# Performance work log

Hardware: AMD Instinct MI355X
Metric: run time of the kernel (lower is better)

The kernel has to match this reference:

```python
import jax, jax.numpy as jnp
import numpy as np

D_MODEL = 768
NHEAD = 12
D_K = D_MODEL // NHEAD
D_FF = 3072
EPS = 1e-6


def layer_norm(x, a, b):
    # torch LayerNorm here: mean/std over last dim, std is UNBIASED (n-1), eps added to std
    n = x.shape[-1]
    m = jnp.mean(x, axis=-1, keepdims=True)
    var = jnp.sum((x - m) ** 2, axis=-1, keepdims=True) / (n - 1)
    return a * (x - m) / (jnp.sqrt(var) + EPS) + b


def setup_inputs() -> dict:
    key = jax.random.key(0)
    ks = jax.random.split(key, 12)
    B, S = 2, 2048
    s = 1.0 / np.sqrt(D_MODEL)
    inp = {
        'x': jax.random.normal(ks[0], (B, S, D_MODEL), jnp.float32),
        'mask': jnp.ones((B, 1, S), jnp.int32),
        'Wq': jax.random.normal(ks[1], (D_MODEL, D_MODEL), jnp.float32) * s,
        'bq': jnp.zeros((D_MODEL,), jnp.float32),
        'Wk': jax.random.normal(ks[2], (D_MODEL, D_MODEL), jnp.float32) * s,
        'bk': jnp.zeros((D_MODEL,), jnp.float32),
        'Wv': jax.random.normal(ks[3], (D_MODEL, D_MODEL), jnp.float32) * s,
        'bv': jnp.zeros((D_MODEL,), jnp.float32),
        'Wo': jax.random.normal(ks[4], (D_MODEL, D_MODEL), jnp.float32) * s,
        'bo': jnp.zeros((D_MODEL,), jnp.float32),
        'ln1_a': jnp.ones((D_MODEL,), jnp.float32),
        'ln1_b': jnp.zeros((D_MODEL,), jnp.float32),
        'W1': jax.random.normal(ks[5], (D_MODEL, D_FF), jnp.float32) * s,
        'b1': jnp.zeros((D_FF,), jnp.float32),
        'W2': jax.random.normal(ks[6], (D_FF, D_MODEL), jnp.float32) * (1.0 / np.sqrt(D_FF)),
        'b2': jnp.zeros((D_MODEL,), jnp.float32),
        'ln2_a': jnp.ones((D_MODEL,), jnp.float32),
        'ln2_b': jnp.zeros((D_MODEL,), jnp.float32),
    }
    return inp


def reference(x, mask, Wq, bq, Wk, bk, Wv, bv, Wo, bo, ln1_a, ln1_b, W1, b1, W2, b2, ln2_a, ln2_b):
    B, S, _ = x.shape
    # --- sublayer 1: pre-norm self-attention + residual (dropout = eval/no-op) ---
    h = layer_norm(x, ln1_a, ln1_b)
    q = (h @ Wq + bq).reshape(B, S, NHEAD, D_K).transpose(0, 2, 1, 3)  # [B,H,S,Dk]
    k = (h @ Wk + bk).reshape(B, S, NHEAD, D_K).transpose(0, 2, 1, 3)
    v = (h @ Wv + bv).reshape(B, S, NHEAD, D_K).transpose(0, 2, 1, 3)
    scores = jnp.einsum('bhqd,bhkd->bhqk', q, k) / np.sqrt(D_K)  # [B,H,S,S]
    scores = jnp.where(mask[:, None] == 0, jnp.float32(-1e9), scores)
    attn = jax.nn.softmax(scores, axis=-1)
    ctx = jnp.einsum('bhqk,bhkd->bhqd', attn, v)  # [B,H,S,Dk]
    ctx = ctx.transpose(0, 2, 1, 3).reshape(B, S, D_MODEL)
    x = x + (ctx @ Wo + bo)
    # --- sublayer 2: pre-norm FFN + residual ---
    h2 = layer_norm(x, ln2_a, ln2_b)
    ff = jax.nn.relu(h2 @ W1 + b1) @ W2 + b2
    return x + ff
```

## Files before the change

kernel.cpp:

```cpp
#include <hip/hip_runtime.h>
#include <hip/hip_bf16.h>
#include <stdint.h>

#define DM 768
#define DFF 3072
#define NH 12
#define DK 64
#define SS 2048
#define NTOK 4096
#define KCH 2

typedef __hip_bfloat16 bf16;
typedef short bf16x8 __attribute__((ext_vector_type(8)));
typedef float f32x4 __attribute__((ext_vector_type(4)));

#define MFMA16(a, b, c) __builtin_amdgcn_mfma_f32_16x16x32_bf16((a), (b), (c), 0, 0, 0)

#define QSCALE 0.18033688011112042f

#if __has_builtin(__builtin_amdgcn_exp2f)
#define EXP2F(x) __builtin_amdgcn_exp2f(x)
#else
#define EXP2F(x) exp2f(x)
#endif

static __device__ __forceinline__ bf16 f2b(float f) { return __float2bfloat16(f); }
static __device__ __forceinline__ unsigned short f2b_bits(float f) {
    bf16 h = __float2bfloat16(f);
    return *reinterpret_cast<unsigned short*>(&h);
}
static __device__ __forceinline__ float b2f(bf16 h) { return __bfloat162float(h); }

static __device__ __forceinline__ void g2l16(const void* g, void* l) {
    __builtin_amdgcn_global_load_lds(
        (const __attribute__((address_space(1))) unsigned int*)g,
        (__attribute__((address_space(3))) unsigned int*)(uintptr_t)l,
        16, 0, 0);
}

__global__ __launch_bounds__(256) void fused_pre(const float* Wq, const float* Wk,
                                                 const float* Wv, const float* Wo,
                                                 const float* W1, const float* W2,
                                                 bf16* WqT, bf16* WkT, bf16* WvT,
                                                 bf16* WoT, bf16* W1T, bf16* W2T,
                                                 const float* __restrict__ x,
                                                 const float* __restrict__ lg,
                                                 const float* __restrict__ lb,
                                                 bf16* __restrict__ hout) {
    int id = blockIdx.x;
    if (id >= 6912) {
        int wid = threadIdx.x >> 6, lane = threadIdx.x & 63;
        int row = (id - 6912) * 4 + wid;
        const float* xr = x + (size_t)row * DM;
        float v[12];
        float s = 0.f;
#pragma unroll
        for (int i = 0; i < 12; ++i) { v[i] = xr[lane + i * 64]; s += v[i]; }
#pragma unroll
        for (int off = 32; off >= 1; off >>= 1) s += __shfl_xor(s, off);
        float mean = s * (1.f / 768.f);
        float s2 = 0.f;
#pragma unroll
        for (int i = 0; i < 12; ++i) { float d = v[i] - mean; s2 += d * d; }
#pragma unroll
        for (int off = 32; off >= 1; off >>= 1) s2 += __shfl_xor(s2, off);
        float rstd = 1.f / (sqrtf(s2 * (1.f / 767.f)) + 1e-6f);
        bf16* orow = hout + (size_t)row * DM;
#pragma unroll
        for (int i = 0; i < 12; ++i) {
            int c = lane + i * 64;
            orow[c] = f2b(lg[c] * (v[i] - mean) * rstd + lb[c]);
        }
        return;
    }
    __shared__ float tile[32][33];
    const float* W; bf16* WT; int K, N, n0, k0;
    if (id < 2304) {
        int z = id / 576, r = id % 576;
        W  = (z == 0) ? Wq : (z == 1) ? Wk : (z == 2) ? Wv : Wo;
        WT = (z == 0) ? WqT : (z == 1) ? WkT : (z == 2) ? WvT : WoT;
        K = 768; N = 768; n0 = (r % 24) * 32; k0 = (r / 24) * 32;
    } else if (id < 4608) {
        int r = id - 2304; W = W1; WT = W1T;
        K = 768; N = 3072; n0 = (r % 96) * 32; k0 = (r / 96) * 32;
    } else {
        int r = id - 4608; W = W2; WT = W2T;
        K = 3072; N = 768; n0 = (r % 24) * 32; k0 = (r / 24) * 32;
    }
    int tx = threadIdx.x & 31, ty = threadIdx.x >> 5;
#pragma unroll
    for (int r = ty; r < 32; r += 8)
        tile[r][tx] = W[(size_t)(k0 + r) * N + n0 + tx];
    __syncthreads();
#pragma unroll
    for (int r = ty; r < 32; r += 8)
        WT[(size_t)(n0 + r) * K + k0 + tx] = f2b(tile[tx][r]);
}

__global__ __launch_bounds__(256) void ln_fwd(const float* __restrict__ x,
                                              const float* __restrict__ g,
                                              const float* __restrict__ be,
                                              bf16* __restrict__ out) {
    int wid = threadIdx.x >> 6, lane = threadIdx.x & 63;
    int row = blockIdx.x * 4 + wid;
    const float* xr = x + (size_t)row * DM;
    float v[12];
    float s = 0.f;
#pragma unroll
    for (int i = 0; i < 12; ++i) { v[i] = xr[lane + i * 64]; s += v[i]; }
#pragma unroll
    for (int off = 32; off >= 1; off >>= 1) s += __shfl_xor(s, off);
    float mean = s * (1.f / 768.f);
    float s2 = 0.f;
#pragma unroll
    for (int i = 0; i < 12; ++i) { float d = v[i] - mean; s2 += d * d; }
#pragma unroll
    for (int off = 32; off >= 1; off >>= 1) s2 += __shfl_xor(s2, off);
    float rstd = 1.f / (sqrtf(s2 * (1.f / 767.f)) + 1e-6f);
    bf16* orow = out + (size_t)row * DM;
#pragma unroll
    for (int i = 0; i < 12; ++i) {
        int c = lane + i * 64;
        orow[c] = f2b(g[c] * (v[i] - mean) * rstd + be[c]);
    }
}

__device__ __forceinline__ void gemm_core(const bf16* __restrict__ A,
                                          const bf16* __restrict__ BT,
                                          int K, int bm, int bn,
                                          bf16* As, bf16* Bs,
                                          f32x4 acc[4][4]) {
    int tid = threadIdx.x;
    int lane = tid & 63, quad = lane >> 4, lid = lane & 15;
    int wid = tid >> 6;
    int wm = (wid >> 1) * 64, wn = (wid & 1) * 64;
    int s0 = tid, s1 = tid + 256;
    int r0 = s0 >> 2, c0 = (s0 & 3) ^ ((r0 >> 1) & 3);
    int r1 = s1 >> 2, c1 = (s1 & 3) ^ ((r1 >> 1) & 3);
    const bf16* A0 = A + (size_t)(bm + r0) * K + c0 * 8;
    const bf16* A1 = A + (size_t)(bm + r1) * K + c1 * 8;
    const bf16* B0 = BT + (size_t)(bn + r0) * K + c0 * 8;
    const bf16* B1 = BT + (size_t)(bn + r1) * K + c1 * 8;
    int rdc = quad ^ ((lid >> 1) & 3);
    g2l16(A0, As + s0 * 8);
    g2l16(B0, Bs + s0 * 8);
    g2l16(A1, As + s1 * 8);
    g2l16(B1, Bs + s1 * 8);
    for (int k0 = 0; k0 < K; k0 += 32) {
        __syncthreads();
        int cur = (k0 >> 5) & 1;
        if (k0 + 32 < K) {
            int nb = (cur ^ 1) * 4096;
            g2l16(A0 + k0 + 32, As + nb + s0 * 8);
            g2l16(B0 + k0 + 32, Bs + nb + s0 * 8);
            g2l16(A1 + k0 + 32, As + nb + s1 * 8);
            g2l16(B1 + k0 + 32, Bs + nb + s1 * 8);
        }
        const bf16* Ac = As + cur * 4096;
        const bf16* Bc = Bs + cur * 4096;
        bf16x8 af[4], bfr[4];
#pragma unroll
        for (int i = 0; i < 4; ++i) af[i]  = *(const bf16x8*)&Ac[(wm + i * 16 + lid) * 32 + rdc * 8];
#pragma unroll
        for (int j = 0; j < 4; ++j) bfr[j] = *(const bf16x8*)&Bc[(wn + j * 16 + lid) * 32 + rdc * 8];
#pragma unroll
        for (int i = 0; i < 4; ++i)
#pragma unroll
            for (int j = 0; j < 4; ++j)
                acc[i][j] = MFMA16(af[i], bfr[j], acc[i][j]);
    }
}

__global__ __launch_bounds__(256) void gemm_qkv(const bf16* __restrict__ A,
                                                const bf16* __restrict__ WqT,
                                                const bf16* __restrict__ WkT,
                                                const bf16* __restrict__ WvT,
                                                const float* __restrict__ bq,
                                                const float* __restrict__ bk,
                                                const float* __restrict__ bv,
                                                bf16* __restrict__ qb,
                                                bf16* __restrict__ kb,
                                                bf16* __restrict__ vtb) {
    __shared__ bf16 As[2 * 128 * 32];
    __shared__ bf16 Bs[2 * 128 * 32];
    int which = blockIdx.x / 6;
    int bn = (blockIdx.x % 6) * 128;
    int bm = blockIdx.y * 128;
    const bf16* BT = (which == 0) ? WqT : (which == 1) ? WkT : WvT;
    const float* bias = (which == 0) ? bq : (which == 1) ? bk : bv;
    f32x4 acc[4][4] = {};
    gemm_core(A, BT, DM, bm, bn, As, Bs, acc);

    int tid = threadIdx.x, wid = tid >> 6, lane = tid & 63, quad = lane >> 4, lid = lane & 15;
    int wm = (wid >> 1) * 64, wn = (wid & 1) * 64;
    float sc = (which == 0) ? QSCALE : 1.f;
#pragma unroll
    for (int j = 0; j < 4; ++j) {
        int col = bn + wn + j * 16 + lid;
        float bb = bias[col];
        int hh = col >> 6, d = col & 63;
#pragma unroll
        for (int i = 0; i < 4; ++i) {
            int rowbase = bm + wm + i * 16 + quad * 4;
            int b = rowbase >> 11;
            int s0 = rowbase & 2047;
            if (which == 2) {
                ushort4 pk;
                pk.x = f2b_bits(acc[i][j][0] + bb);
                pk.y = f2b_bits(acc[i][j][1] + bb);
                pk.z = f2b_bits(acc[i][j][2] + bb);
                pk.w = f2b_bits(acc[i][j][3] + bb);
                *(ushort4*)&vtb[(((size_t)b * NH + hh) * DK + d) * SS + s0] = pk;
            } else {
                bf16* dst = which ? kb : qb;
#pragma unroll
                for (int r = 0; r < 4; ++r)
                    dst[(((size_t)b * NH + hh) * SS + (s0 + r)) * DK + d] = f2b((acc[i][j][r] + bb) * sc);
            }
        }
    }
}

template <int EPI>
__global__ __launch_bounds__(256) void gemm_ep(const bf16* __restrict__ A,
                                               const bf16* __restrict__ BT,
                                               const float* __restrict__ bias,
                                               const float* __restrict__ res,
                                               void* __restrict__ outp,
                                               int N, int K) {
    __shared__ bf16 As[2 * 128 * 32];
    __shared__ bf16 Bs[2 * 128 * 32];
    int bm = blockIdx.y * 128, bn = blockIdx.x * 128;
    f32x4 acc[4][4] = {};
    gemm_core(A, BT, K, bm, bn, As, Bs, acc);

    int tid = threadIdx.x, wid = tid >> 6, lane = tid & 63, quad = lane >> 4, lid = lane & 15;
    int wm = (wid >> 1) * 64, wn = (wid & 1) * 64;
#pragma unroll
    for (int j = 0; j < 4; ++j) {
        int col = bn + wn + j * 16 + lid;
        float bb = bias[col];
#pragma unroll
        for (int i = 0; i < 4; ++i) {
#pragma unroll
            for (int r = 0; r < 4; ++r) {
                int row = bm + wm + i * 16 + quad * 4 + r;
                float v = acc[i][j][r] + bb;
                if (EPI == 2) {
                    ((float*)outp)[(size_t)row * N + col] = res[(size_t)row * N + col] + v;
                } else {
                    ((bf16*)outp)[(size_t)row * N + col] = f2b(fmaxf(v, 0.f));
                }
            }
        }
    }
}

template <int EPI>
__global__ __launch_bounds__(256) void gemm_ep96(const bf16* __restrict__ A,
                                                 const bf16* __restrict__ BT,
                                                 const float* __restrict__ bias,
                                                 const float* __restrict__ res,
                                                 void* __restrict__ outp,
                                                 int N, int K) {
    __shared__ bf16 As[2 * 64 * 32];
    __shared__ bf16 Bs[2 * 96 * 32];
    int bm = blockIdx.y * 64, bn = blockIdx.x * 96;
    int tid = threadIdx.x, wid = tid >> 6, lane = tid & 63, quad = lane >> 4, lid = lane & 15;
    int wm = (wid >> 1) * 32, wn = (wid & 1) * 48;
    f32x4 acc[2][3] = {};
    int ra = tid >> 2, ca = (tid & 3) ^ ((ra >> 1) & 3);
    int s0 = tid, s1 = tid + 256;
    int rb0 = s0 >> 2, cb0 = (s0 & 3) ^ ((rb0 >> 1) & 3);
    int rb1 = s1 >> 2, cb1 = (s1 & 3) ^ ((rb1 >> 1) & 3);
    const bf16* Ap = A + (size_t)(bm + ra) * K + ca * 8;
    const bf16* B0 = BT + (size_t)(bn + rb0) * K + cb0 * 8;
    const bf16* B1 = BT + (size_t)(bn + rb1) * K + cb1 * 8;
    int rdc = quad ^ ((lid >> 1) & 3);
    bool doB1 = tid < 128;
    g2l16(Ap, As + tid * 8);
    g2l16(B0, Bs + s0 * 8);
    if (doB1) g2l16(B1, Bs + s1 * 8);
    for (int k0 = 0; k0 < K; k0 += 32) {
        __syncthreads();
        int cur = (k0 >> 5) & 1;
        if (k0 + 32 < K) {
            g2l16(Ap + k0 + 32, As + (cur ^ 1) * 2048 + tid * 8);
            g2l16(B0 + k0 + 32, Bs + (cur ^ 1) * 3072 + s0 * 8);
            if (doB1) g2l16(B1 + k0 + 32, Bs + (cur ^ 1) * 3072 + s1 * 8);
        }
        const bf16* Ac = As + cur * 2048;
        const bf16* Bc = Bs + cur * 3072;
        bf16x8 af[2], bfr[3];
#pragma unroll
        for (int i = 0; i < 2; ++i) af[i]  = *(const bf16x8*)&Ac[(wm + i * 16 + lid) * 32 + rdc * 8];
#pragma unroll
        for (int j = 0; j < 3; ++j) bfr[j] = *(const bf16x8*)&Bc[(wn + j * 16 + lid) * 32 + rdc * 8];
#pragma unroll
        for (int i = 0; i < 2; ++i)
#pragma unroll
            for (int j = 0; j < 3; ++j)
                acc[i][j] = MFMA16(af[i], bfr[j], acc[i][j]);
    }
#pragma unroll
    for (int j = 0; j < 3; ++j) {
        int col = bn + wn + j * 16 + lid;
        float bb = bias[col];
#pragma unroll
        for (int i = 0; i < 2; ++i) {
#pragma unroll
            for (int r = 0; r < 4; ++r) {
                int row = bm + wm + i * 16 + quad * 4 + r;
                float v = acc[i][j][r] + bb;
                if (EPI == 2) {
                    ((float*)outp)[(size_t)row * N + col] = res[(size_t)row * N + col] + v;
                } else {
                    ((bf16*)outp)[(size_t)row * N + col] = f2b(fmaxf(v, 0.f));
                }
            }
        }
    }
}

__global__ __launch_bounds__(256) void attn_part(const bf16* __restrict__ qb,
                                                 const bf16* __restrict__ kb,
                                                 const bf16* __restrict__ vtb,
                                                 const int* __restrict__ mask,
                                                 bf16* __restrict__ part,
                                                 float* __restrict__ lws) {
    __shared__ bf16 Ks[2 * 64 * 64];
    __shared__ bf16 VTs[2 * 64 * 64];
    __shared__ bf16 Ps[128 * 72];
    int bh = blockIdx.y;
    int b = bh / NH;
    int q0 = blockIdx.x * 128;
    int kc = blockIdx.z;
    const bf16* Kp = kb  + (size_t)bh * SS * DK;
    const bf16* VT = vtb + (size_t)bh * DK * SS;
    int tid = threadIdx.x, wid = tid >> 6, lane = tid & 63, quad = lane >> 4, lid = lane & 15;

    int s0 = tid, s1 = tid + 256;
    int r0 = s0 >> 3, c0 = (s0 & 7) ^ (r0 & 7);
    int r1 = s1 >> 3, c1 = (s1 & 7) ^ (r1 & 7);

    const int* mrow = mask + b * SS;
    int tbeg = kc * (SS / 64 / KCH), tend = (kc + 1) * (SS / 64 / KCH);

    int myfull;
    {
        const int4* m4 = (const int4*)(mrow + tbeg * 64);
        int4 mm = m4[tid];
        myfull = (mm.x != 0) & (mm.y != 0) & (mm.z != 0) & (mm.w != 0);
    }
    int blockfull = __syncthreads_and(myfull);

    bf16x8 qf0[2], qf1[2];
#pragma unroll
    for (int u = 0; u < 2; ++u) {
        const bf16* Qrow = qb + ((size_t)bh * SS + q0 + wid * 32 + u * 16 + lid) * DK;
        qf0[u] = *(const bf16x8*)&Qrow[quad * 8];
        qf1[u] = *(const bf16x8*)&Qrow[32 + quad * 8];
    }

    bf16x8 ones;
#pragma unroll
    for (int i = 0; i < 8; ++i) ones[i] = (short)0x3F80;

    int rdc  = quad ^ (lid & 7);
    int rdc2 = rdc ^ 4;

    f32x4 accv[2][4] = {};
    f32x4 accl[2] = {};

    {
        int k0 = tbeg * 64;
        g2l16(Kp + (size_t)(k0 + r0) * DK + c0 * 8, Ks + s0 * 8);
        g2l16(Kp + (size_t)(k0 + r1) * DK + c1 * 8, Ks + s1 * 8);
        g2l16(VT + (size_t)r0 * SS + k0 + c0 * 8, VTs + s0 * 8);
        g2l16(VT + (size_t)r1 * SS + k0 + c1 * 8, VTs + s1 * 8);
    }

    int cur = 0;
    for (int t = tbeg; t < tend; ++t) {
        int k0 = t * 64;
        __syncthreads();
        if (t + 1 < tend) {
            int k0n = (t + 1) * 64;
            int nb = (cur ^ 1) * 4096;
            g2l16(Kp + (size_t)(k0n + r0) * DK + c0 * 8, Ks + nb + s0 * 8);
            g2l16(Kp + (size_t)(k0n + r1) * DK + c1 * 8, Ks + nb + s1 * 8);
            g2l16(VT + (size_t)r0 * SS + k0n + c0 * 8, VTs + nb + s0 * 8);
            g2l16(VT + (size_t)r1 * SS + k0n + c1 * 8, VTs + nb + s1 * 8);
        }
        const bf16* Kc  = Ks  + cur * 4096;
        const bf16* VTc = VTs + cur * 4096;

#pragma unroll
        for (int ns = 0; ns < 4; ++ns) {
            bf16x8 kf0 = *(const bf16x8*)&Kc[(ns * 16 + lid) * 64 + rdc * 8];
            bf16x8 kf1 = *(const bf16x8*)&Kc[(ns * 16 + lid) * 64 + rdc2 * 8];
#pragma unroll
            for (int u = 0; u < 2; ++u) {
                f32x4 st = {};
                st = MFMA16(kf0, qf0[u], st);
                st = MFMA16(kf1, qf1[u], st);
                float p0, p1, p2, p3;
                if (blockfull) {
                    p0 = EXP2F(st[0]);
                    p1 = EXP2F(st[1]);
                    p2 = EXP2F(st[2]);
                    p3 = EXP2F(st[3]);
                } else {
                    int4 mk = *(const int4*)&mrow[k0 + ns * 16 + quad * 4];
                    p0 = mk.x ? EXP2F(st[0]) : 0.f;
                    p1 = mk.y ? EXP2F(st[1]) : 0.f;
                    p2 = mk.z ? EXP2F(st[2]) : 0.f;
                    p3 = mk.w ? EXP2F(st[3]) : 0.f;
                }
                __hip_bfloat162 h01 = __float22bfloat162_rn(make_float2(p0, p1));
                __hip_bfloat162 h23 = __float22bfloat162_rn(make_float2(p2, p3));
                uint2 pw;
                pw.x = *(unsigned int*)&h01;
                pw.y = *(unsigned int*)&h23;
                *(uint2*)&Ps[(wid * 32 + u * 16 + lid) * 72 + ns * 16 + quad * 4] = pw;
            }
        }

        bf16x8 pa0[2], pa1[2];
#pragma unroll
        for (int u = 0; u < 2; ++u) {
            pa0[u] = *(const bf16x8*)&Ps[(wid * 32 + u * 16 + lid) * 72 + quad * 8];
            pa1[u] = *(const bf16x8*)&Ps[(wid * 32 + u * 16 + lid) * 72 + 32 + quad * 8];
            accl[u] = MFMA16(pa0[u], ones, accl[u]);
            accl[u] = MFMA16(pa1[u], ones, accl[u]);
        }

#pragma unroll
        for (int ds = 0; ds < 4; ++ds) {
            bf16x8 vf0 = *(const bf16x8*)&VTc[(ds * 16 + lid) * 64 + rdc * 8];
            bf16x8 vf1 = *(const bf16x8*)&VTc[(ds * 16 + lid) * 64 + rdc2 * 8];
#pragma unroll
            for (int u = 0; u < 2; ++u) {
                accv[u][ds] = MFMA16(pa0[u], vf0, accv[u][ds]);
                accv[u][ds] = MFMA16(pa1[u], vf1, accv[u][ds]);
            }
        }
        cur ^= 1;
    }

    bf16* pb = part + ((size_t)kc * (2 * NH) + bh) * DK * SS;
#pragma unroll
    for (int u = 0; u < 2; ++u) {
        if (lid == 0) {
#pragma unroll
            for (int r = 0; r < 4; ++r)
                lws[((size_t)kc * (2 * NH) + bh) * SS + q0 + wid * 32 + u * 16 + quad * 4 + r] = accl[u][r];
        }
        int qbase = q0 + wid * 32 + u * 16 + quad * 4;
#pragma unroll
        for (int ds = 0; ds < 4; ++ds) {
            int d = ds * 16 + lid;
            ushort4 pk;
            pk.x = f2b_bits(accv[u][ds][0]);
            pk.y = f2b_bits(accv[u][ds][1]);
            pk.z = f2b_bits(accv[u][ds][2]);
            pk.w = f2b_bits(accv[u][ds][3]);
            *(ushort4*)&pb[(size_t)d * SS + qbase] = pk;
        }
    }
}

__global__ __launch_bounds__(256) void attn_combine(const bf16* __restrict__ part,
                                                    const float* __restrict__ lws,
                                                    bf16* __restrict__ ctx) {
    __shared__ float tile[64][66];
    __shared__ float linv[64];
    int bh = blockIdx.y;
    int b = bh / NH, h = bh % NH;
    int q0 = blockIdx.x * 64;
    int tid = threadIdx.x;

    if (tid < 64) {
        float l = 0.f;
#pragma unroll
        for (int kc = 0; kc < KCH; ++kc)
            l += lws[((size_t)kc * (2 * NH) + bh) * SS + q0 + tid];
        linv[tid] = 1.f / l;
    }

    int d = tid >> 2, qs = (tid & 3) * 16;
    const bf16* p0 = part + (((size_t)0 * (2 * NH) + bh) * DK + d) * SS + q0 + qs;
    const bf16* p1 = part + (((size_t)1 * (2 * NH) + bh) * DK + d) * SS + q0 + qs;
    bf16x8 a0 = *(const bf16x8*)p0;
    bf16x8 a1 = *(const bf16x8*)(p0 + 8);
    bf16x8 b0 = *(const bf16x8*)p1;
    bf16x8 b1 = *(const bf16x8*)(p1 + 8);
#pragma unroll
    for (int i = 0; i < 8; ++i) {
        tile[d][qs + i]     = b2f(((const bf16*)&a0)[i]) + b2f(((const bf16*)&b0)[i]);
        tile[d][qs + 8 + i] = b2f(((const bf16*)&a1)[i]) + b2f(((const bf16*)&b1)[i]);
    }
    __syncthreads();

    int q = tid >> 2, ds2 = (tid & 3) * 16;
    float rl = linv[q];
    unsigned int wv[8];
#pragma unroll
    for (int i = 0; i < 8; ++i) {
        __hip_bfloat162 hh = __float22bfloat162_rn(
            make_float2(tile[ds2 + 2 * i][q] * rl, tile[ds2 + 2 * i + 1][q] * rl));
        wv[i] = *(unsigned int*)&hh;
    }
    bf16* crow = ctx + (size_t)(b * SS + q0 + q) * DM + h * DK + ds2;
    uint4 u0 = {wv[0], wv[1], wv[2], wv[3]};
    uint4 u1 = {wv[4], wv[5], wv[6], wv[7]};
    *(uint4*)&crow[0] = u0;
    *(uint4*)&crow[8] = u1;
}

extern "C" void kernel_launch(void* const* d_in, const int* in_sizes, int n_in,
                              void* d_out, int out_size, void* d_ws, size_t ws_size,
                              hipStream_t stream) {
    const float* x    = (const float*)d_in[0];
    const int*   mask = (const int*)d_in[1];
    const float* Wq   = (const float*)d_in[2];
    const float* bq   = (const float*)d_in[3];
    const float* Wk   = (const float*)d_in[4];
    const float* bk   = (const float*)d_in[5];
    const float* Wv   = (const float*)d_in[6];
    const float* bv   = (const float*)d_in[7];
    const float* Wo   = (const float*)d_in[8];
    const float* bo   = (const float*)d_in[9];
    const float* ln1a = (const float*)d_in[10];
    const float* ln1b = (const float*)d_in[11];
    const float* W1   = (const float*)d_in[12];
    const float* b1   = (const float*)d_in[13];
    const float* W2   = (const float*)d_in[14];
    const float* b2   = (const float*)d_in[15];
    const float* ln2a = (const float*)d_in[16];
    const float* ln2b = (const float*)d_in[17];
    float* out = (float*)d_out;

    char* w = (char*)d_ws;
    bf16* h   = (bf16*)w; w += (size_t)NTOK * DM * 2;
    bf16* qb  = (bf16*)w; w += (size_t)NTOK * DM * 2;
    bf16* kb  = (bf16*)w; w += (size_t)NTOK * DM * 2;
    bf16* vtb = (bf16*)w; w += (size_t)NTOK * DM * 2;
    bf16* ctx = (bf16*)w; w += (size_t)NTOK * DM * 2;
    bf16* h2  = (bf16*)w; w += (size_t)NTOK * DM * 2;
    bf16* ffa = (bf16*)w; w += (size_t)NTOK * DFF * 2;
    float* x1 = (float*)w; w += (size_t)NTOK * DM * 4;
    bf16* WqT = (bf16*)w; w += (size_t)DM * DM * 2;
    bf16* WkT = (bf16*)w; w += (size_t)DM * DM * 2;
    bf16* WvT = (bf16*)w; w += (size_t)DM * DM * 2;
    bf16* WoT = (bf16*)w; w += (size_t)DM * DM * 2;
    bf16* W1T = (bf16*)w; w += (size_t)DM * DFF * 2;
    bf16* W2T = (bf16*)w; w += (size_t)DM * DFF * 2;

    bf16*  part = ffa;
    float* lws  = x1;

    fused_pre<<<6912 + NTOK / 4, 256, 0, stream>>>(Wq, Wk, Wv, Wo, W1, W2,
                                                   WqT, WkT, WvT, WoT, W1T, W2T,
                                                   x, ln1a, ln1b, h);
    gemm_qkv<<<dim3(18, 32), 256, 0, stream>>>(h, WqT, WkT, WvT, bq, bk, bv, qb, kb, vtb);
    attn_part<<<dim3(SS / 128, 2 * NH, KCH), 256, 0, stream>>>(qb, kb, vtb, mask, part, lws);
    attn_combine<<<dim3(SS / 64, 2 * NH), 256, 0, stream>>>(part, lws, ctx);
    gemm_ep96<2><<<dim3(8, 64), 256, 0, stream>>>(ctx, WoT, bo, x, (void*)x1, DM, DM);
    ln_fwd<<<NTOK / 4, 256, 0, stream>>>(x1, ln2a, ln2b, h2);
    gemm_ep<3><<<dim3(24, 32), 256, 0, stream>>>(h2, W1T, b1, nullptr, (void*)ffa, DFF, DM);
    gemm_ep96<2><<<dim3(8, 64), 256, 0, stream>>>(ffa, W2T, b2, x1, (void*)out, DM, DFF);
}
```

Before: 287.0 us.

## Retile QKV GEMM, add split-K W2 GEMM, and XCD-swizzle block order

The QKV projection now uses 128x96 tiles with an inlined double-buffered loop, giving 768 blocks instead of 576 for better CU fill. The W2 GEMM (K=3072) moves to a new 512-thread kernel that splits K between two half-blocks and reduces their partials through LDS, using 64x128 tiles. Block indices are remapped so consecutive tiles land on the same XCD, which is meant to improve L2 reuse. The cost is an extra LDS reduction and more sync in the W2 kernel.

```diff
diff --git a/kernel.cpp b/kernel.cpp
--- a/kernel.cpp
+++ b/kernel.cpp
@@ -36,6 +36,11 @@
         (const __attribute__((address_space(1))) unsigned int*)g,
         (__attribute__((address_space(3))) unsigned int*)(uintptr_t)l,
         16, 0, 0);
+}
+
+static __device__ __forceinline__ int xcd_swz(int bid, int nwg) {
+    int q = nwg >> 3;
+    return (bid & 7) * q + (bid >> 3);
 }
 
 __global__ __launch_bounds__(256) void fused_pre(const float* Wq, const float* Wk,
@@ -182,20 +187,57 @@
                                                 bf16* __restrict__ kb,
                                                 bf16* __restrict__ vtb) {
     __shared__ bf16 As[2 * 128 * 32];
-    __shared__ bf16 Bs[2 * 128 * 32];
-    int which = blockIdx.x / 6;
-    int bn = (blockIdx.x % 6) * 128;
-    int bm = blockIdx.y * 128;
+    __shared__ bf16 Bs[2 * 96 * 32];
+    int wg = xcd_swz(blockIdx.x, 768);
+    int bnx = wg % 24;
+    int bm = (wg / 24) * 128;
+    int which = bnx / 8;
+    int bn = (bnx % 8) * 96;
     const bf16* BT = (which == 0) ? WqT : (which == 1) ? WkT : WvT;
     const float* bias = (which == 0) ? bq : (which == 1) ? bk : bv;
-    f32x4 acc[4][4] = {};
-    gemm_core(A, BT, DM, bm, bn, As, Bs, acc);
 
     int tid = threadIdx.x, wid = tid >> 6, lane = tid & 63, quad = lane >> 4, lid = lane & 15;
-    int wm = (wid >> 1) * 64, wn = (wid & 1) * 64;
+    int wm = (wid >> 1) * 64, wn = (wid & 1) * 48;
+    f32x4 acc[4][3] = {};
+    int s0 = tid, s1 = tid + 256;
+    int r0 = s0 >> 2, c0 = (s0 & 3) ^ ((r0 >> 1) & 3);
+    int r1 = s1 >> 2, c1 = (s1 & 3) ^ ((r1 >> 1) & 3);
+    const bf16* A0 = A + (size_t)(bm + r0) * DM + c0 * 8;
+    const bf16* A1 = A + (size_t)(bm + r1) * DM + c1 * 8;
+    const bf16* B0 = BT + (size_t)(bn + r0) * DM + c0 * 8;
+    const bf16* B1 = BT + (size_t)(bn + r1) * DM + c1 * 8;
+    int rdc = quad ^ ((lid >> 1) & 3);
+    bool doB1 = tid < 128;
+    g2l16(A0, As + s0 * 8);
+    g2l16(A1, As + s1 * 8);
+    g2l16(B0, Bs + s0 * 8);
+    if (doB1) g2l16(B1, Bs + s1 * 8);
+    for (int k0 = 0; k0 < DM; k0 += 32) {
+        __syncthreads();
+        int cur = (k0 >> 5) & 1;
+        if (k0 + 32 < DM) {
+            g2l16(A0 + k0 + 32, As + (cur ^ 1) * 4096 + s0 * 8);
+            g2l16(A1 + k0 + 32, As + (cur ^ 1) * 4096 + s1 * 8);
+            g2l16(B0 + k0 + 32, Bs + (cur ^ 1) * 3072 + s0 * 8);
+            if (doB1) g2l16(B1 + k0 + 32, Bs + (cur ^ 1) * 3072 + s1 * 8);
+        }
+        const bf16* Ac = As + cur * 4096;
+        const bf16* Bc = Bs + cur * 3072;
+        bf16x8 af[4], bfr[3];
+#pragma unroll
+        for (int i = 0; i < 4; ++i) af[i]  = *(const bf16x8*)&Ac[(wm + i * 16 + lid) * 32 + rdc * 8];
+#pragma unroll
+        for (int j = 0; j < 3; ++j) bfr[j] = *(const bf16x8*)&Bc[(wn + j * 16 + lid) * 32 + rdc * 8];
+#pragma unroll
+        for (int i = 0; i < 4; ++i)
+#pragma unroll
+            for (int j = 0; j < 3; ++j)
+                acc[i][j] = MFMA16(af[i], bfr[j], acc[i][j]);
+    }
+
     float sc = (which == 0) ? QSCALE : 1.f;
 #pragma unroll
-    for (int j = 0; j < 4; ++j) {
+    for (int j = 0; j < 3; ++j) {
         int col = bn + wn + j * 16 + lid;
         float bb = bias[col];
         int hh = col >> 6, d = col & 63;
@@ -203,19 +245,19 @@
         for (int i = 0; i < 4; ++i) {
             int rowbase = bm + wm + i * 16 + quad * 4;
             int b = rowbase >> 11;
-            int s0 = rowbase & 2047;
+            int s0r = rowbase & 2047;
             if (which == 2) {
                 ushort4 pk;
                 pk.x = f2b_bits(acc[i][j][0] + bb);
                 pk.y = f2b_bits(acc[i][j][1] + bb);
                 pk.z = f2b_bits(acc[i][j][2] + bb);
                 pk.w = f2b_bits(acc[i][j][3] + bb);
-                *(ushort4*)&vtb[(((size_t)b * NH + hh) * DK + d) * SS + s0] = pk;
+                *(ushort4*)&vtb[(((size_t)b * NH + hh) * DK + d) * SS + s0r] = pk;
             } else {
                 bf16* dst = which ? kb : qb;
 #pragma unroll
                 for (int r = 0; r < 4; ++r)
-                    dst[(((size_t)b * NH + hh) * SS + (s0 + r)) * DK + d] = f2b((acc[i][j][r] + bb) * sc);
+                    dst[(((size_t)b * NH + hh) * SS + (s0r + r)) * DK + d] = f2b((acc[i][j][r] + bb) * sc);
             }
         }
     }
@@ -257,6 +299,98 @@
 }
 
 template <int EPI>
+__global__ __launch_bounds__(512) void gemm_ep64(const bf16* __restrict__ A,
+                                                 const bf16* __restrict__ BT,
+                                                 const float* __restrict__ bias,
+                                                 const float* __restrict__ res,
+                                                 void* __restrict__ outp,
+                                                 int N, int K) {
+    __shared__ char smem[49152];
+    int tid = threadIdx.x;
+    int half = tid >> 8, htid = tid & 255;
+    bf16* As = (bf16*)smem + half * 4096;
+    bf16* Bs = (bf16*)(smem + 16384) + half * 8192;
+    int K2 = K >> 1, koff = half * K2;
+    int wg = xcd_swz(blockIdx.x, gridDim.x);
+    int bm = (wg / 6) * 64, bn = (wg % 6) * 128;
+    int wid = htid >> 6, lane = tid & 63, quad = lane >> 4, lid = lane & 15;
+    int wm = (wid >> 1) * 32, wn = (wid & 1) * 64;
+    f32x4 acc[2][4] = {};
+    int ra = htid >> 2, ca = (htid & 3) ^ ((ra >> 1) & 3);
+    int s0 = htid, s1 = htid + 256;
+    int rb0 = s0 >> 2, cb0 = (s0 & 3) ^ ((rb0 >> 1) & 3);
+    int rb1 = s1 >> 2, cb1 = (s1 & 3) ^ ((rb1 >> 1) & 3);
+    const bf16* Ap = A + (size_t)(bm + ra) * K + koff + ca * 8;
+    const bf16* B0 = BT + (size_t)(bn + rb0) * K + koff + cb0 * 8;
+    const bf16* B1 = BT + (size_t)(bn + rb1) * K + koff + cb1 * 8;
+    int rdc = quad ^ ((lid >> 1) & 3);
+    g2l16(Ap, As + htid * 8);
+    g2l16(B0, Bs + s0 * 8);
+    g2l16(B1, Bs + s1 * 8);
+    for (int k0 = 0; k0 < K2; k0 += 32) {
+        __syncthreads();
+        int cur = (k0 >> 5) & 1;
+        if (k0 + 32 < K2) {
+            g2l16(Ap + k0 + 32, As + (cur ^ 1) * 2048 + htid * 8);
+            g2l16(B0 + k0 + 32, Bs + (cur ^ 1) * 4096 + s0 * 8);
+            g2l16(B1 + k0 + 32, Bs + (cur ^ 1) * 4096 + s1 * 8);
+        }
+        const bf16* Ac = As + cur * 2048;
+        const bf16* Bc = Bs + cur * 4096;
+        bf16x8 af[2], bfr[4];
+#pragma unroll
+        for (int i = 0; i < 2; ++i) af[i]  = *(const bf16x8*)&Ac[(wm + i * 16 + lid) * 32 + rdc * 8];
+#pragma unroll
+        for (int j = 0; j < 4; ++j) bfr[j] = *(const bf16x8*)&Bc[(wn + j * 16 + lid) * 32 + rdc * 8];
+#pragma unroll
+        for (int i = 0; i < 2; ++i)
+#pragma unroll
+            for (int j = 0; j < 4; ++j)
+                acc[i][j] = MFMA16(af[i], bfr[j], acc[i][j]);
+    }
+    __syncthreads();
+    float* red = (float*)smem;
+    if (half == 1) {
+#pragma unroll
+        for (int i = 0; i < 2; ++i)
+#pragma unroll
+            for (int j = 0; j < 4; ++j) {
+                int c = i * 4 + j;
+                *(f32x4*)&red[htid * 32 + ((c ^ (htid & 7)) << 2)] = acc[i][j];
+            }
+    }
+    __syncthreads();
+    if (half == 0) {
+#pragma unroll
+        for (int i = 0; i < 2; ++i)
+#pragma unroll
+            for (int j = 0; j < 4; ++j) {
+                int c = i * 4 + j;
+                f32x4 o = *(const f32x4*)&red[htid * 32 + ((c ^ (htid & 7)) << 2)];
+                acc[i][j] += o;
+            }
+#pragma unroll
+        for (int j = 0; j < 4; ++j) {
+            int col = bn + wn + j * 16 + lid;
+            float bb = bias[col];
+#pragma unroll
+            for (int i = 0; i < 2; ++i) {
+#pragma unroll
+                for (int r = 0; r < 4; ++r) {
+                    int row = bm + wm + i * 16 + quad * 4 + r;
+                    float v = acc[i][j][r] + bb;
+                    if (EPI == 2) {
+                        ((float*)outp)[(size_t)row * N + col] = res[(size_t)row * N + col] + v;
+                    } else {
+                        ((bf16*)outp)[(size_t)row * N + col] = f2b(fmaxf(v, 0.f));
+                    }
+                }
+            }
+        }
+    }
+}
+
+template <int EPI>
 __global__ __launch_bounds__(256) void gemm_ep96(const bf16* __restrict__ A,
                                                  const bf16* __restrict__ BT,
                                                  const float* __restrict__ bias,
@@ -265,7 +399,8 @@
                                                  int N, int K) {
     __shared__ bf16 As[2 * 64 * 32];
     __shared__ bf16 Bs[2 * 96 * 32];
-    int bm = blockIdx.y * 64, bn = blockIdx.x * 96;
+    int wg = xcd_swz(blockIdx.x, gridDim.x);
+    int bm = (wg / 8) * 64, bn = (wg % 8) * 96;
     int tid = threadIdx.x, wid = tid >> 6, lane = tid & 63, quad = lane >> 4, lid = lane & 15;
     int wm = (wid >> 1) * 32, wn = (wid & 1) * 48;
     f32x4 acc[2][3] = {};
@@ -563,11 +698,11 @@
     fused_pre<<<6912 + NTOK / 4, 256, 0, stream>>>(Wq, Wk, Wv, Wo, W1, W2,
                                                    WqT, WkT, WvT, WoT, W1T, W2T,
                                                    x, ln1a, ln1b, h);
-    gemm_qkv<<<dim3(18, 32), 256, 0, stream>>>(h, WqT, WkT, WvT, bq, bk, bv, qb, kb, vtb);
+    gemm_qkv<<<768, 256, 0, stream>>>(h, WqT, WkT, WvT, bq, bk, bv, qb, kb, vtb);
     attn_part<<<dim3(SS / 128, 2 * NH, KCH), 256, 0, stream>>>(qb, kb, vtb, mask, part, lws);
     attn_combine<<<dim3(SS / 64, 2 * NH), 256, 0, stream>>>(part, lws, ctx);
-    gemm_ep96<2><<<dim3(8, 64), 256, 0, stream>>>(ctx, WoT, bo, x, (void*)x1, DM, DM);
+    gemm_ep96<2><<<512, 256, 0, stream>>>(ctx, WoT, bo, x, (void*)x1, DM, DM);
     ln_fwd<<<NTOK / 4, 256, 0, stream>>>(x1, ln2a, ln2b, h2);
     gemm_ep<3><<<dim3(24, 32), 256, 0, stream>>>(h2, W1T, b1, nullptr, (void*)ffa, DFF, DM);
-    gemm_ep96<2><<<dim3(8, 64), 256, 0, stream>>>(ffa, W2T, b2, x1, (void*)out, DM, DFF);
-}
+    gemm_ep64<2><<<384, 512, 0, stream>>>(ffa, W2T, b2, x1, (void*)out, DM, DFF);
+}
```

After: 272.8 us. -4.9%, faster.
